# Performance work log

Hardware: AMD Instinct MI355X
Metric: run time of the kernel (lower is better)

The kernel has to match this reference:

```python
import jax, jax.numpy as jnp
import numpy as np

N_NODES = 100000
N_EDGES = 400000
IN_DIM = 69        # torchdrug default atom feature dim
HIDDEN = 256
NUM_CLASSES = 2
NUM_GRAPHS = 4096


def gcn_conv(x, W, b, src, dst, n_nodes):
    """PyG GCNConv: out = D^{-1/2}(A+I)D^{-1/2} (x W) + b (self-loops added)."""
    h = x @ W  # [N, out_dim]
    loop = jnp.arange(n_nodes, dtype=src.dtype)
    s = jnp.concatenate([src, loop])  # sources incl. self loops
    d = jnp.concatenate([dst, loop])  # targets incl. self loops
    deg = jax.ops.segment_sum(jnp.ones_like(d, dtype=h.dtype), d, num_segments=n_nodes)
    dinv = jnp.where(deg > 0, jax.lax.rsqrt(deg), 0.0)
    norm = dinv[s] * dinv[d]  # [E+N]
    msgs = h[s] * norm[:, None]  # gather + scale
    out = jax.ops.segment_sum(msgs, d, num_segments=n_nodes)  # scatter-add
    return out + b


def setup_inputs() -> dict:
    key = jax.random.key(0)
    ks = jax.random.split(key, 16)
    x = jax.random.normal(ks[0], (N_NODES, IN_DIM), dtype=jnp.float32)
    edge_index = jax.random.randint(ks[1], (2, N_EDGES), 0, N_NODES, dtype=jnp.int64)
    batch = jnp.sort(jax.random.randint(ks[2], (N_NODES,), 0, NUM_GRAPHS, dtype=jnp.int64))

    def glorot(k, fan_in, fan_out):
        lim = np.sqrt(6.0 / (fan_in + fan_out)).astype(np.float32)
        return jax.random.uniform(k, (fan_in, fan_out), jnp.float32, -lim, lim)

    W1 = glorot(ks[3], IN_DIM, HIDDEN)
    W2 = glorot(ks[4], HIDDEN, HIDDEN)
    W3 = glorot(ks[5], HIDDEN, HIDDEN)
    W4 = glorot(ks[6], HIDDEN, HIDDEN)
    b1 = jnp.zeros((HIDDEN,), jnp.float32)
    b2 = jnp.zeros((HIDDEN,), jnp.float32)
    b3 = jnp.zeros((HIDDEN,), jnp.float32)
    b4 = jnp.zeros((HIDDEN,), jnp.float32)
    Wl = glorot(ks[7], HIDDEN, NUM_CLASSES)
    bl = jnp.zeros((NUM_CLASSES,), jnp.float32)
    return {"x": x, "edge_index": edge_index, "batch": batch,
            "W1": W1, "b1": b1, "W2": W2, "b2": b2,
            "W3": W3, "b3": b3, "W4": W4, "b4": b4,
            "Wl": Wl, "bl": bl}


def reference(x, edge_index, batch, W1, b1, W2, b2, W3, b3, W4, b4, Wl, bl):
    src, dst = edge_index[0], edge_index[1]
    n = x.shape[0]
    h = jax.nn.relu(gcn_conv(x, W1, b1, src, dst, n))
    h = jax.nn.relu(gcn_conv(h, W2, b2, src, dst, n))
    h = jax.nn.relu(gcn_conv(h, W3, b3, src, dst, n))
    h = gcn_conv(h, W4, b4, src, dst, n)
    # global_mean_pool
    sums = jax.ops.segment_sum(h, batch, num_segments=NUM_GRAPHS)  # [G, H]
    cnts = jax.ops.segment_sum(jnp.ones((n,), h.dtype), batch, num_segments=NUM_GRAPHS)
    pooled = sums / jnp.maximum(cnts, 1.0)[:, None]
    # dropout is identity in eval mode
    return pooled @ Wl + bl  # [G, num_classes]
```

## Files before the change

kernel.cpp:

```cpp
#include <hip/hip_runtime.h>
#include <hip/hip_bf16.h>

#define N_NODES 100000
#define M_PAD   100096
#define N_EDGES 400000
#define IN_DIM  69
#define KPX     96
#define KPA     128
#define HID     256
#define NG      4096
#define SCAN_B  391
#define FILL_B  1563

typedef __attribute__((ext_vector_type(8))) short bf16x8;
typedef __attribute__((ext_vector_type(4))) float f32x4;
typedef unsigned short u16;
typedef unsigned int   u32;

__device__ __forceinline__ float b2f(u16 v) {
    u32 x = ((u32)v) << 16;
    return __builtin_bit_cast(float, x);
}
__device__ __forceinline__ u16 f2b(float f) {
    u32 x = __builtin_bit_cast(u32, f);
    u32 r = (x + 0x7FFF + ((x >> 16) & 1)) >> 16;
    return (u16)r;
}
__device__ __forceinline__ float lo16(u32 v) { return b2f((u16)(v & 0xffff)); }
__device__ __forceinline__ float hi16(u32 v) { return b2f((u16)(v >> 16)); }

__device__ __forceinline__ void acc8(float* a, uint4 w, float m) {
    a[0] = fmaf(m, lo16(w.x), a[0]); a[1] = fmaf(m, hi16(w.x), a[1]);
    a[2] = fmaf(m, lo16(w.y), a[2]); a[3] = fmaf(m, hi16(w.y), a[3]);
    a[4] = fmaf(m, lo16(w.z), a[4]); a[5] = fmaf(m, hi16(w.z), a[5]);
    a[6] = fmaf(m, lo16(w.w), a[6]); a[7] = fmaf(m, hi16(w.w), a[7]);
}
__device__ __forceinline__ void acc4(float* a, uint2 w, float m) {
    a[0] = fmaf(m, lo16(w.x), a[0]); a[1] = fmaf(m, hi16(w.x), a[1]);
    a[2] = fmaf(m, lo16(w.y), a[2]); a[3] = fmaf(m, hi16(w.y), a[3]);
}

__device__ __forceinline__ void gl_lds16(const u16* g, u16* l) {
    __builtin_amdgcn_global_load_lds(
        (const __attribute__((address_space(1))) void*)g,
        (__attribute__((address_space(3))) void*)l, 16, 0, 0);
}

__global__ void k_deg(const int* __restrict__ dst, int* __restrict__ deg) {
    int e = blockIdx.x * blockDim.x + threadIdx.x;
    if (e < N_EDGES) atomicAdd(&deg[dst[e]], 1);
}

__global__ void k_scan_local(const int* __restrict__ deg, int* __restrict__ rowptr,
                             int* __restrict__ bsum, float* __restrict__ dinv) {
    __shared__ int s[256];
    int tid = threadIdx.x;
    int i = blockIdx.x * 256 + tid;
    int v = (i < N_NODES) ? deg[i] : 0;
    if (i < N_NODES) dinv[i] = rsqrtf((float)v + 1.0f);
    s[tid] = v;
    __syncthreads();
    #pragma unroll
    for (int off = 1; off < 256; off <<= 1) {
        int t = 0;
        if (tid >= off) t = s[tid - off];
        __syncthreads();
        if (tid >= off) s[tid] += t;
        __syncthreads();
    }
    if (i < N_NODES) rowptr[i] = s[tid] - v;
    if (tid == 255) bsum[blockIdx.x] = s[255];
}

__global__ void k_scan_bsum(int* __restrict__ bsum, int* __restrict__ boff) {
    __shared__ int s[512];
    int tid = threadIdx.x;
    int v = (tid < SCAN_B) ? bsum[tid] : 0;
    s[tid] = v;
    __syncthreads();
    #pragma unroll
    for (int off = 1; off < 512; off <<= 1) {
        int t = 0;
        if (tid >= off) t = s[tid - off];
        __syncthreads();
        if (tid >= off) s[tid] += t;
        __syncthreads();
    }
    if (tid < SCAN_B) boff[tid] = s[tid] - v;
}

__global__ void k_scan_add(int* __restrict__ rowptr, const int* __restrict__ boff) {
    int i = blockIdx.x * 256 + threadIdx.x;
    if (i < N_NODES) rowptr[i] += boff[blockIdx.x];
    if (i == 0) rowptr[N_NODES] = N_EDGES;
}

__global__ __launch_bounds__(256) void k_fill_pad(const int* __restrict__ src,
                       const int* __restrict__ dst,
                       const int* __restrict__ rowptr, int* __restrict__ fill,
                       int* __restrict__ col,
                       const float* __restrict__ x, const float* __restrict__ dinv,
                       u16* __restrict__ xs) {
    if (blockIdx.x < FILL_B) {
        int e = blockIdx.x * 256 + threadIdx.x;
        if (e < N_EDGES) {
            int d = dst[e];
            int pos = rowptr[d] + atomicAdd(&fill[d], 1);
            col[pos] = src[e];
        }
    } else {
        int node = (blockIdx.x - FILL_B) * 4 + (threadIdx.x >> 6);
        if (node >= N_NODES) return;
        int lane = threadIdx.x & 63;
        if (lane >= 48) return;
        int d0 = lane * 2, d1 = lane * 2 + 1;
        float dv = dinv[node];
        const float* xr = x + (size_t)node * IN_DIM;
        float v0 = (d0 < IN_DIM) ? xr[d0] * dv : 0.0f;
        float v1 = (d1 < IN_DIM) ? xr[d1] * dv : 0.0f;
        u32 o = (u32)f2b(v0) | ((u32)f2b(v1) << 16);
        *(u32*)(xs + (size_t)node * KPX + d0) = o;
    }
}

__global__ void k_prep(const float* __restrict__ W1, const float* __restrict__ W2,
                       const float* __restrict__ W3, const float* __restrict__ W4,
                       const float* __restrict__ Wl, const float* __restrict__ b4,
                       const float* __restrict__ bl, const int* __restrict__ batch,
                       u16* __restrict__ Wt1, u16* __restrict__ Wt2, u16* __restrict__ Wt3,
                       float* __restrict__ W4l, float* __restrict__ c4, int* __restrict__ gptr) {
    int b = blockIdx.x;
    int t = threadIdx.x;
    if (b < KPA) {
        Wt1[(size_t)t * KPA + b] = (b < IN_DIM) ? f2b(W1[(size_t)b * HID + t]) : (u16)0;
    } else if (b < KPA + HID) {
        int k = b - KPA;
        Wt2[(size_t)t * HID + k] = f2b(W2[(size_t)k * HID + t]);
    } else if (b < KPA + 2 * HID) {
        int k = b - KPA - HID;
        Wt3[(size_t)t * HID + k] = f2b(W3[(size_t)k * HID + t]);
    } else if (b == KPA + 2 * HID) {
        float s0 = 0.0f, s1 = 0.0f;
        const float* wr = W4 + (size_t)t * HID;
        for (int j = 0; j < HID; ++j) {
            float w = wr[j];
            s0 += w * Wl[j * 2 + 0];
            s1 += w * Wl[j * 2 + 1];
        }
        W4l[t * 2 + 0] = s0;
        W4l[t * 2 + 1] = s1;
        if (t < 2) {
            float s = bl[t];
            for (int j = 0; j < HID; ++j) s += b4[j] * Wl[j * 2 + t];
            c4[t] = s;
        }
    } else {
        int g = (b - (KPA + 2 * HID + 1)) * 256 + t;
        if (g > NG) return;
        if (g == NG) { gptr[NG] = N_NODES; return; }
        int lo = 0, hi = N_NODES;
        while (lo < hi) {
            int mid = (lo + hi) >> 1;
            if (batch[mid] < g) lo = mid + 1; else hi = mid;
        }
        gptr[g] = lo;
    }
}

__global__ __launch_bounds__(256) void k_agg96(const int* __restrict__ rowptr,
                                               const int* __restrict__ col,
                                               const u16* __restrict__ xs,
                                               const float* __restrict__ dinv,
                                               u16* __restrict__ xa) {
    int node = blockIdx.x * 8 + (threadIdx.x >> 5);
    if (node >= N_NODES) return;
    int l = threadIdx.x & 31;
    int j = l * 4;
    if (l >= 24) {
        *(uint2*)(xa + (size_t)node * KPA + j) = make_uint2(0, 0);
        return;
    }
    const u16* xj = xs + j;
    float a[4];
    {
        uint2 v = *(const uint2*)(xj + (size_t)node * KPX);
        a[0] = lo16(v.x); a[1] = hi16(v.x); a[2] = lo16(v.y); a[3] = hi16(v.y);
    }
    int e = rowptr[node], end = rowptr[node + 1];
    for (; e < end; e += 8) {
        int idx[8]; float mm[8];
        #pragma unroll
        for (int u = 0; u < 8; ++u) {
            int ee = e + u;
            idx[u] = (ee < end) ? ee : e;
            mm[u]  = (ee < end) ? 1.0f : 0.0f;
        }
        mm[0] = 1.0f;
        uint2 w[8];
        #pragma unroll
        for (int u = 0; u < 8; ++u) w[u] = *(const uint2*)(xj + (size_t)col[idx[u]] * KPX);
        #pragma unroll
        for (int u = 0; u < 8; ++u) acc4(a, w[u], mm[u]);
    }
    float dv = dinv[node];
    uint2 o;
    o.x = (u32)f2b(a[0] * dv) | ((u32)f2b(a[1] * dv) << 16);
    o.y = (u32)f2b(a[2] * dv) | ((u32)f2b(a[3] * dv) << 16);
    *(uint2*)(xa + (size_t)node * KPA + j) = o;
}

template<int MODE>
__global__ __launch_bounds__(256) void k_gemm(const u16* __restrict__ A, int KP,
                                              const u16* __restrict__ Wt,
                                              const float* __restrict__ dinv,
                                              const float* __restrict__ bias,
                                              u16* __restrict__ Out) {
    __shared__ __align__(16) u16 As[128 * 64];
    __shared__ __align__(16) u16 Bs[128 * 64];

    const int tid  = threadIdx.x;
    const int wave = tid >> 6;
    const int lane = tid & 63;
    const int quad = lane >> 4;
    const int lm   = lane & 15;
    const int wr   = wave >> 1;
    const int wc   = wave & 1;
    const int m0   = blockIdx.x * 128;
    const int n0   = blockIdx.y * 128;

    f32x4 acc[4][4] = {};

    const int sr = lane >> 3;
    const int sc = lane & 7;
    const int gc = sc ^ (sr & 7);

    for (int kt = 0; kt < KP; kt += 64) {
        __syncthreads();
        #pragma unroll
        for (int i = 0; i < 4; ++i) {
            int s = wave * 4 + i;
            int r = s * 8 + sr;
            const u16* ga = A  + (size_t)(m0 + r) * KP + kt + gc * 8;
            const u16* gb = Wt + (size_t)(n0 + r) * KP + kt + gc * 8;
            gl_lds16(ga, As + s * 512);
            gl_lds16(gb, Bs + s * 512);
        }
        __syncthreads();

        #pragma unroll
        for (int st = 0; st < 2; ++st) {
            bf16x8 af[4], bfr[4];
            const int slot = ((st * 4 + quad) ^ (lm & 7)) * 8;
            #pragma unroll
            for (int rt = 0; rt < 4; ++rt)
                af[rt] = *(const bf16x8*)(As + (wr * 64 + rt * 16 + lm) * 64 + slot);
            #pragma unroll
            for (int ct = 0; ct < 4; ++ct)
                bfr[ct] = *(const bf16x8*)(Bs + (wc * 64 + ct * 16 + lm) * 64 + slot);
            #pragma unroll
            for (int rt = 0; rt < 4; ++rt)
                #pragma unroll
                for (int ct = 0; ct < 4; ++ct)
                    acc[rt][ct] = __builtin_amdgcn_mfma_f32_16x16x32_bf16(af[rt], bfr[ct], acc[rt][ct], 0, 0, 0);
        }
    }

    #pragma unroll
    for (int rt = 0; rt < 4; ++rt) {
        #pragma unroll
        for (int reg = 0; reg < 4; ++reg) {
            int m = m0 + wr * 64 + rt * 16 + quad * 4 + reg;
            if (m >= N_NODES) continue;
            float dv = (MODE == 0) ? dinv[m] : 0.0f;
            #pragma unroll
            for (int ct = 0; ct < 4; ++ct) {
                int n = n0 + wc * 64 + ct * 16 + lm;
                float v = acc[rt][ct][reg];
                if (MODE == 0) v *= dv;
                else           v = fmaxf(v + bias[n], 0.0f);
                Out[(size_t)m * HID + n] = f2b(v);
            }
        }
    }
}

__global__ __launch_bounds__(256) void k_agg256(const int* __restrict__ rowptr,
                                                const int* __restrict__ col,
                                                const u16* __restrict__ g,
                                                const float* __restrict__ dinv,
                                                const float* __restrict__ bias,
                                                u16* __restrict__ Xout) {
    int node = blockIdx.x * 8 + (threadIdx.x >> 5);
    if (node >= N_NODES) return;
    int l = threadIdx.x & 31;
    int j = l * 8;
    const u16* gj = g + j;

    float a[8];
    {
        uint4 v = *(const uint4*)(gj + (size_t)node * HID);
        a[0] = lo16(v.x); a[1] = hi16(v.x); a[2] = lo16(v.y); a[3] = hi16(v.y);
        a[4] = lo16(v.z); a[5] = hi16(v.z); a[6] = lo16(v.w); a[7] = hi16(v.w);
    }
    int e = rowptr[node], end = rowptr[node + 1];
    for (; e < end; e += 8) {
        int idx[8]; float mm[8];
        #pragma unroll
        for (int u = 0; u < 8; ++u) {
            int ee = e + u;
            idx[u] = (ee < end) ? ee : e;
            mm[u]  = (ee < end) ? 1.0f : 0.0f;
        }
        mm[0] = 1.0f;
        uint4 w[8];
        #pragma unroll
        for (int u = 0; u < 8; ++u) w[u] = *(const uint4*)(gj + (size_t)col[idx[u]] * HID);
        #pragma unroll
        for (int u = 0; u < 8; ++u) acc8(a, w[u], mm[u]);
    }
    float dv = dinv[node];
    float4 b0 = *(const float4*)(bias + j);
    float4 b1 = *(const float4*)(bias + j + 4);
    float r0 = fmaxf(fmaf(a[0], dv, b0.x), 0.0f);
    float r1 = fmaxf(fmaf(a[1], dv, b0.y), 0.0f);
    float r2 = fmaxf(fmaf(a[2], dv, b0.z), 0.0f);
    float r3 = fmaxf(fmaf(a[3], dv, b0.w), 0.0f);
    float r4 = fmaxf(fmaf(a[4], dv, b1.x), 0.0f);
    float r5 = fmaxf(fmaf(a[5], dv, b1.y), 0.0f);
    float r6 = fmaxf(fmaf(a[6], dv, b1.z), 0.0f);
    float r7 = fmaxf(fmaf(a[7], dv, b1.w), 0.0f);
    uint4 o;
    o.x = (u32)f2b(r0) | ((u32)f2b(r1) << 16);
    o.y = (u32)f2b(r2) | ((u32)f2b(r3) << 16);
    o.z = (u32)f2b(r4) | ((u32)f2b(r5) << 16);
    o.w = (u32)f2b(r6) | ((u32)f2b(r7) << 16);
    *(uint4*)(Xout + (size_t)node * HID + j) = o;
}

__global__ __launch_bounds__(256) void k_agg_head(const int* __restrict__ rowptr,
                                                  const int* __restrict__ col,
                                                  const u16* __restrict__ g,
                                                  const float* __restrict__ dinv,
                                                  const float* __restrict__ bias,
                                                  const float* __restrict__ W4l,
                                                  float* __restrict__ g4) {
    __shared__ float2 sW[HID];
    sW[threadIdx.x] = *(const float2*)(W4l + threadIdx.x * 2);
    __syncthreads();

    int node = blockIdx.x * 8 + (threadIdx.x >> 5);
    if (node >= N_NODES) return;
    int l = threadIdx.x & 31;
    int j = l * 8;
    const u16* gj = g + j;

    float a[8];
    {
        uint4 v = *(const uint4*)(gj + (size_t)node * HID);
        a[0] = lo16(v.x); a[1] = hi16(v.x); a[2] = lo16(v.y); a[3] = hi16(v.y);
        a[4] = lo16(v.z); a[5] = hi16(v.z); a[6] = lo16(v.w); a[7] = hi16(v.w);
    }
    int e = rowptr[node], end = rowptr[node + 1];
    for (; e < end; e += 8) {
        int idx[8]; float mm[8];
        #pragma unroll
        for (int u = 0; u < 8; ++u) {
            int ee = e + u;
            idx[u] = (ee < end) ? ee : e;
            mm[u]  = (ee < end) ? 1.0f : 0.0f;
        }
        mm[0] = 1.0f;
        uint4 w[8];
        #pragma unroll
        for (int u = 0; u < 8; ++u) w[u] = *(const uint4*)(gj + (size_t)col[idx[u]] * HID);
        #pragma unroll
        for (int u = 0; u < 8; ++u) acc8(a, w[u], mm[u]);
    }
    float dv = dinv[node];
    float4 b0 = *(const float4*)(bias + j);
    float4 b1 = *(const float4*)(bias + j + 4);
    float r[8];
    r[0] = fmaxf(fmaf(a[0], dv, b0.x), 0.0f);
    r[1] = fmaxf(fmaf(a[1], dv, b0.y), 0.0f);
    r[2] = fmaxf(fmaf(a[2], dv, b0.z), 0.0f);
    r[3] = fmaxf(fmaf(a[3], dv, b0.w), 0.0f);
    r[4] = fmaxf(fmaf(a[4], dv, b1.x), 0.0f);
    r[5] = fmaxf(fmaf(a[5], dv, b1.y), 0.0f);
    r[6] = fmaxf(fmaf(a[6], dv, b1.z), 0.0f);
    r[7] = fmaxf(fmaf(a[7], dv, b1.w), 0.0f);
    float s0 = 0.0f, s1 = 0.0f;
    #pragma unroll
    for (int i = 0; i < 8; ++i) {
        float2 w = sW[j + i];
        s0 = fmaf(r[i], w.x, s0);
        s1 = fmaf(r[i], w.y, s1);
    }
    #pragma unroll
    for (int off = 16; off >= 1; off >>= 1) {
        s0 += __shfl_down(s0, off, 32);
        s1 += __shfl_down(s1, off, 32);
    }
    if (l == 0)
        *(float2*)(g4 + (size_t)node * 2) = make_float2(s0 * dv, s1 * dv);
}

__global__ void k_agg2(const int* __restrict__ rowptr, const int* __restrict__ col,
                       const float* __restrict__ g4, const float* __restrict__ dinv,
                       float* __restrict__ h4) {
    int node = blockIdx.x * blockDim.x + threadIdx.x;
    if (node >= N_NODES) return;
    float2 a = *(const float2*)(g4 + (size_t)node * 2);
    int e = rowptr[node], end = rowptr[node + 1];
    for (; e < end; ++e) {
        float2 w = *(const float2*)(g4 + (size_t)col[e] * 2);
        a.x += w.x; a.y += w.y;
    }
    float dv = dinv[node];
    *(float2*)(h4 + (size_t)node * 2) = make_float2(a.x * dv, a.y * dv);
}

__global__ __launch_bounds__(256) void k_pool2(const float* __restrict__ h4,
                                               const int* __restrict__ gptr,
                                               const float* __restrict__ c4,
                                               float* __restrict__ out) {
    int gph = blockIdx.x * 4 + (threadIdx.x >> 6);
    if (gph >= NG) return;
    int lane = threadIdx.x & 63;
    int b = gptr[gph], e = gptr[gph + 1];
    float s0 = 0.0f, s1 = 0.0f;
    for (int n = b + lane; n < e; n += 64) {
        float2 v = *(const float2*)(h4 + (size_t)n * 2);
        s0 += v.x; s1 += v.y;
    }
    #pragma unroll
    for (int off = 32; off >= 1; off >>= 1) {
        s0 += __shfl_down(s0, off);
        s1 += __shfl_down(s1, off);
    }
    if (lane == 0) {
        float inv = 1.0f / fmaxf((float)(e - b), 1.0f);
        out[gph * 2 + 0] = s0 * inv + c4[0];
        out[gph * 2 + 1] = s1 * inv + c4[1];
    }
}

extern "C" void kernel_launch(void* const* d_in, const int* in_sizes, int n_in,
                              void* d_out, int out_size, void* d_ws, size_t ws_size,
                              hipStream_t stream) {
    const float* x   = (const float*)d_in[0];
    const int* ei    = (const int*)d_in[1];
    const int* src   = ei;
    const int* dst   = ei + N_EDGES;
    const int* batch = (const int*)d_in[2];
    const float* W1 = (const float*)d_in[3];  const float* b1 = (const float*)d_in[4];
    const float* W2 = (const float*)d_in[5];  const float* b2 = (const float*)d_in[6];
    const float* W3 = (const float*)d_in[7];  const float* b3 = (const float*)d_in[8];
    const float* W4 = (const float*)d_in[9];  const float* b4 = (const float*)d_in[10];
    const float* Wl = (const float*)d_in[11]; const float* bl = (const float*)d_in[12];
    float* out = (float*)d_out;

    char* p = (char*)d_ws;
    auto take = [&](size_t bytes) { char* r = p; p += (bytes + 255) & ~(size_t)255; return r; };
    size_t zbytes = (size_t)(N_NODES + N_NODES) * 4;
    int*   deg  = (int*)take(zbytes);
    int*   fill = deg + N_NODES;
    float* dinv = (float*)take((size_t)N_NODES * sizeof(float));
    int* rowptr = (int*)take((size_t)(N_NODES + 1) * sizeof(int));
    int* col    = (int*)take((size_t)N_EDGES * sizeof(int));
    int* bsum   = (int*)take((size_t)SCAN_B * sizeof(int));
    int* boff   = (int*)take((size_t)SCAN_B * sizeof(int));
    int* gptr   = (int*)take((size_t)(NG + 1) * sizeof(int));
    float* W4l  = (float*)take((size_t)HID * 2 * sizeof(float));
    float* c4   = (float*)take(2 * sizeof(float));
    float* g4   = (float*)take((size_t)N_NODES * 2 * sizeof(float));
    float* h4   = (float*)take((size_t)N_NODES * 2 * sizeof(float));
    u16* Wt1 = (u16*)take((size_t)HID * KPA * 2);
    u16* Wt2 = (u16*)take((size_t)HID * HID * 2);
    u16* Wt3 = (u16*)take((size_t)HID * HID * 2);
    u16* Xs  = (u16*)take((size_t)N_NODES * KPX * 2);
    u16* Xa  = (u16*)take((size_t)M_PAD * KPA * 2);
    u16* Gbuf = (u16*)take((size_t)N_NODES * HID * 2);
    u16* Xbuf = (u16*)take((size_t)M_PAD * HID * 2);

    hipMemsetAsync(deg, 0, zbytes, stream);

    k_deg<<<(N_EDGES + 255) / 256, 256, 0, stream>>>(dst, deg);
    k_scan_local<<<SCAN_B, 256, 0, stream>>>(deg, rowptr, bsum, dinv);
    k_scan_bsum<<<1, 512, 0, stream>>>(bsum, boff);
    k_scan_add<<<SCAN_B, 256, 0, stream>>>(rowptr, boff);
    k_fill_pad<<<FILL_B + (N_NODES + 3) / 4, 256, 0, stream>>>(src, dst, rowptr, fill, col,
                                                               x, dinv, Xs);
    k_prep<<<KPA + 2 * HID + 1 + (NG + 256) / 256, 256, 0, stream>>>(
        W1, W2, W3, W4, Wl, b4, bl, batch, Wt1, Wt2, Wt3, W4l, c4, gptr);

    const int nb8 = (N_NODES + 7) / 8;
    const dim3 gemm_grid(M_PAD / 128, HID / 128);

    k_agg96<<<nb8, 256, 0, stream>>>(rowptr, col, Xs, dinv, Xa);
    k_gemm<1><<<gemm_grid, 256, 0, stream>>>(Xa, KPA, Wt1, dinv, b1, Xbuf);
    k_gemm<0><<<gemm_grid, 256, 0, stream>>>(Xbuf, HID, Wt2, dinv, b2, Gbuf);
    k_agg256<<<nb8, 256, 0, stream>>>(rowptr, col, Gbuf, dinv, b2, Xbuf);
    k_gemm<0><<<gemm_grid, 256, 0, stream>>>(Xbuf, HID, Wt3, dinv, b3, Gbuf);
    k_agg_head<<<nb8, 256, 0, stream>>>(rowptr, col, Gbuf, dinv, b3, W4l, g4);
    k_agg2<<<(N_NODES + 255) / 256, 256, 0, stream>>>(rowptr, col, g4, dinv, h4);
    k_pool2<<<(NG + 3) / 4, 256, 0, stream>>>(h4, gptr, c4, out);
}
```

Measured before the change: 377.0 us.

## Enlarge GEMM M tile to 256 rows and fuse last aggregation into pooling

The bf16 MFMA GEMM now computes a 256x128 output tile per block. It loads two A sub-tiles that share one B tile in LDS, so each B fragment is reused twice and the grid is halved. Separately, the final 2-wide aggregation kernel is folded into the per-graph mean-pool kernel, which removes the h4 buffer round trip and one launch. The cost is a doubled accumulator register footprint and more LDS per block, which can lower occupancy. The fused tail also runs with fewer, longer-running threads.

Result: slower. 454.3 us (+20.5%).

```diff
diff --git a/kernel.cpp b/kernel.cpp
--- a/kernel.cpp
+++ b/kernel.cpp
@@ -215,8 +215,7 @@
                                               const float* __restrict__ dinv,
                                               const float* __restrict__ bias,
                                               u16* __restrict__ Out) {
-    __shared__ __align__(16) u16 As[128 * 64];
-    __shared__ __align__(16) u16 Bs[128 * 64];
+    __shared__ __align__(16) u16 S[3 * 128 * 64];
 
     const int tid  = threadIdx.x;
     const int wave = tid >> 6;
@@ -225,10 +224,10 @@
     const int lm   = lane & 15;
     const int wr   = wave >> 1;
     const int wc   = wave & 1;
-    const int m0   = blockIdx.x * 128;
+    const int m0   = blockIdx.x * 256;
     const int n0   = blockIdx.y * 128;
 
-    f32x4 acc[4][4] = {};
+    f32x4 acc[2][4][4] = {};
 
     const int sr = lane >> 3;
     const int sc = lane & 7;
@@ -240,45 +239,51 @@
         for (int i = 0; i < 4; ++i) {
             int s = wave * 4 + i;
             int r = s * 8 + sr;
-            const u16* ga = A  + (size_t)(m0 + r) * KP + kt + gc * 8;
-            const u16* gb = Wt + (size_t)(n0 + r) * KP + kt + gc * 8;
-            gl_lds16(ga, As + s * 512);
-            gl_lds16(gb, Bs + s * 512);
+            gl_lds16(A  + (size_t)(m0 + r) * KP + kt + gc * 8,       S + s * 512);
+            gl_lds16(A  + (size_t)(m0 + 128 + r) * KP + kt + gc * 8, S + 8192 + s * 512);
+            gl_lds16(Wt + (size_t)(n0 + r) * KP + kt + gc * 8,       S + 16384 + s * 512);
         }
         __syncthreads();
 
         #pragma unroll
         for (int st = 0; st < 2; ++st) {
-            bf16x8 af[4], bfr[4];
+            bf16x8 a0[4], a1[4], bb[4];
             const int slot = ((st * 4 + quad) ^ (lm & 7)) * 8;
             #pragma unroll
-            for (int rt = 0; rt < 4; ++rt)
-                af[rt] = *(const bf16x8*)(As + (wr * 64 + rt * 16 + lm) * 64 + slot);
+            for (int rt = 0; rt < 4; ++rt) {
+                a0[rt] = *(const bf16x8*)(S + (wr * 64 + rt * 16 + lm) * 64 + slot);
+                a1[rt] = *(const bf16x8*)(S + 8192 + (wr * 64 + rt * 16 + lm) * 64 + slot);
+            }
             #pragma unroll
             for (int ct = 0; ct < 4; ++ct)
-                bfr[ct] = *(const bf16x8*)(Bs + (wc * 64 + ct * 16 + lm) * 64 + slot);
+                bb[ct] = *(const bf16x8*)(S + 16384 + (wc * 64 + ct * 16 + lm) * 64 + slot);
             #pragma unroll
             for (int rt = 0; rt < 4; ++rt)
                 #pragma unroll
-                for (int ct = 0; ct < 4; ++ct)
-                    acc[rt][ct] = __builtin_amdgcn_mfma_f32_16x16x32_bf16(af[rt], bfr[ct], acc[rt][ct], 0, 0, 0);
+                for (int ct = 0; ct < 4; ++ct) {
+                    acc[0][rt][ct] = __builtin_amdgcn_mfma_f32_16x16x32_bf16(a0[rt], bb[ct], acc[0][rt][ct], 0, 0, 0);
+                    acc[1][rt][ct] = __builtin_amdgcn_mfma_f32_16x16x32_bf16(a1[rt], bb[ct], acc[1][rt][ct], 0, 0, 0);
+                }
         }
     }
 
     #pragma unroll
-    for (int rt = 0; rt < 4; ++rt) {
-        #pragma unroll
-        for (int reg = 0; reg < 4; ++reg) {
-            int m = m0 + wr * 64 + rt * 16 + quad * 4 + reg;
-            if (m >= N_NODES) continue;
-            float dv = (MODE == 0) ? dinv[m] : 0.0f;
+    for (int mt = 0; mt < 2; ++mt) {
+        #pragma unroll
+        for (int rt = 0; rt < 4; ++rt) {
             #pragma unroll
-            for (int ct = 0; ct < 4; ++ct) {
-                int n = n0 + wc * 64 + ct * 16 + lm;
-                float v = acc[rt][ct][reg];
-                if (MODE == 0) v *= dv;
-                else           v = fmaxf(v + bias[n], 0.0f);
-                Out[(size_t)m * HID + n] = f2b(v);
+            for (int reg = 0; reg < 4; ++reg) {
+                int m = m0 + mt * 128 + wr * 64 + rt * 16 + quad * 4 + reg;
+                if (m >= N_NODES) continue;
+                float dv = (MODE == 0) ? dinv[m] : 0.0f;
+                #pragma unroll
+                for (int ct = 0; ct < 4; ++ct) {
+                    int n = n0 + wc * 64 + ct * 16 + lm;
+                    float v = acc[mt][rt][ct][reg];
+                    if (MODE == 0) v *= dv;
+                    else           v = fmaxf(v + bias[n], 0.0f);
+                    Out[(size_t)m * HID + n] = f2b(v);
+                }
             }
         }
     }
@@ -404,33 +409,28 @@
         *(float2*)(g4 + (size_t)node * 2) = make_float2(s0 * dv, s1 * dv);
 }
 
-__global__ void k_agg2(const int* __restrict__ rowptr, const int* __restrict__ col,
-                       const float* __restrict__ g4, const float* __restrict__ dinv,
-                       float* __restrict__ h4) {
-    int node = blockIdx.x * blockDim.x + threadIdx.x;
-    if (node >= N_NODES) return;
-    float2 a = *(const float2*)(g4 + (size_t)node * 2);
-    int e = rowptr[node], end = rowptr[node + 1];
-    for (; e < end; ++e) {
-        float2 w = *(const float2*)(g4 + (size_t)col[e] * 2);
-        a.x += w.x; a.y += w.y;
-    }
-    float dv = dinv[node];
-    *(float2*)(h4 + (size_t)node * 2) = make_float2(a.x * dv, a.y * dv);
-}
-
-__global__ __launch_bounds__(256) void k_pool2(const float* __restrict__ h4,
-                                               const int* __restrict__ gptr,
-                                               const float* __restrict__ c4,
-                                               float* __restrict__ out) {
+__global__ __launch_bounds__(256) void k_tail(const int* __restrict__ rowptr,
+                                              const int* __restrict__ col,
+                                              const float* __restrict__ g4,
+                                              const float* __restrict__ dinv,
+                                              const int* __restrict__ gptr,
+                                              const float* __restrict__ c4,
+                                              float* __restrict__ out) {
     int gph = blockIdx.x * 4 + (threadIdx.x >> 6);
     if (gph >= NG) return;
     int lane = threadIdx.x & 63;
     int b = gptr[gph], e = gptr[gph + 1];
     float s0 = 0.0f, s1 = 0.0f;
     for (int n = b + lane; n < e; n += 64) {
-        float2 v = *(const float2*)(h4 + (size_t)n * 2);
-        s0 += v.x; s1 += v.y;
+        float2 a = *(const float2*)(g4 + (size_t)n * 2);
+        int ee = rowptr[n], eend = rowptr[n + 1];
+        for (; ee < eend; ++ee) {
+            float2 w = *(const float2*)(g4 + (size_t)col[ee] * 2);
+            a.x += w.x; a.y += w.y;
+        }
+        float dv = dinv[n];
+        s0 = fmaf(a.x, dv, s0);
+        s1 = fmaf(a.y, dv, s1);
     }
     #pragma unroll
     for (int off = 32; off >= 1; off >>= 1) {
@@ -473,7 +473,6 @@
     float* W4l  = (float*)take((size_t)HID * 2 * sizeof(float));
     float* c4   = (float*)take(2 * sizeof(float));
     float* g4   = (float*)take((size_t)N_NODES * 2 * sizeof(float));
-    float* h4   = (float*)take((size_t)N_NODES * 2 * sizeof(float));
     u16* Wt1 = (u16*)take((size_t)HID * KPA * 2);
     u16* Wt2 = (u16*)take((size_t)HID * HID * 2);
     u16* Wt3 = (u16*)take((size_t)HID * HID * 2);
@@ -494,7 +493,7 @@
         W1, W2, W3, W4, Wl, b4, bl, batch, Wt1, Wt2, Wt3, W4l, c4, gptr);
 
     const int nb8 = (N_NODES + 7) / 8;
-    const dim3 gemm_grid(M_PAD / 128, HID / 128);
+    const dim3 gemm_grid(M_PAD / 256, HID / 128);
 
     k_agg96<<<nb8, 256, 0, stream>>>(rowptr, col, Xs, dinv, Xa);
     k_gemm<1><<<gemm_grid, 256, 0, stream>>>(Xa, KPA, Wt1, dinv, b1, Xbuf);
@@ -502,6 +501,5 @@
     k_agg256<<<nb8, 256, 0, stream>>>(rowptr, col, Gbuf, dinv, b2, Xbuf);
     k_gemm<0><<<gemm_grid, 256, 0, stream>>>(Xbuf, HID, Wt3, dinv, b3, Gbuf);
     k_agg_head<<<nb8, 256, 0, stream>>>(rowptr, col, Gbuf, dinv, b3, W4l, g4);
-    k_agg2<<<(N_NODES + 255) / 256, 256, 0, stream>>>(rowptr, col, g4, dinv, h4);
-    k_pool2<<<(NG + 3) / 4, 256, 0, stream>>>(h4, gptr, c4, out);
-}
+    k_tail<<<(NG + 3) / 4, 256, 0, stream>>>(rowptr, col, g4, dinv, gptr, c4, out);
+}
```
